# Kernel optimization log

Hardware: AMD Instinct MI355X
Metric: run time of the kernel (lower is better)

## Reference

```python
import jax, jax.numpy as jnp
import numpy as np

B, S, D_IN, D_E, H = 512, 100, 300, 150, 2  # batch, patches, patch feat, embed half, heads
L = S + 1  # 101 tokens with class token
EPS = 1e-5


def setup_inputs() -> dict:
    key = jax.random.key(0)
    ks = jax.random.split(key, 12)
    r = lambda k, shp, s=0.02: (jax.random.normal(k, shp, jnp.float32) * s)
    return {
        "x": jax.random.normal(ks[0], (B, S, D_IN), jnp.float32),
        "Wp": r(ks[1], (D_IN, D_E)), "bp": jnp.zeros((D_E,), jnp.float32),
        "pos_table": r(ks[2], (L, D_E), 1.0),
        "class_embed": r(ks[3], (D_E,), 1.0),
        "Wq": r(ks[4], (H, 2 * D_E, 2 * D_E)),
        "Wk": r(ks[5], (H, 2 * D_E, 2 * D_E)),
        "Wv": r(ks[6], (H, 2 * D_E, 2 * D_E)),
        "bn1_g": jnp.ones((L,), jnp.float32), "bn1_b": jnp.zeros((L,), jnp.float32),
        "Wp1": r(ks[7], (900, 300)), "bp1": jnp.zeros((300,), jnp.float32),
        "bn2_g": jnp.ones((L,), jnp.float32), "bn2_b": jnp.zeros((L,), jnp.float32),
        "fc1_W": r(ks[8], (1200, 512)), "fc1_b": jnp.zeros((512,), jnp.float32),
        "fc2_W": r(ks[9], (512, 2)), "fc2_b": jnp.zeros((2,), jnp.float32),
    }


def _batchnorm(x, g, b):
    # torch BatchNorm1d(101) on [B, 101, F]: normalize per channel (dim 1) over (B, F), training-mode batch stats
    mean = jnp.mean(x, axis=(0, 2), keepdims=True)
    var = jnp.var(x, axis=(0, 2), keepdims=True)
    return (x - mean) * jax.lax.rsqrt(var + EPS) * g[None, :, None] + b[None, :, None]


def reference(x, Wp, bp, pos_table, class_embed, Wq, Wk, Wv, bn1_g, bn1_b,
              Wp1, bp1, bn2_g, bn2_b, fc1_W, fc1_b, fc2_W, fc2_b):
    h = jax.nn.relu(x @ Wp + bp)                                   # [B,100,150]
    cls = jnp.concatenate([jnp.broadcast_to(class_embed, (B, D_E)),
                           jnp.broadcast_to(pos_table[0], (B, D_E))], axis=-1)   # [B,300]
    tok = jnp.concatenate([h, jnp.broadcast_to(pos_table[1:], (B, S, D_E))], axis=-1)  # [B,100,300]
    z = jnp.concatenate([cls[:, None, :], tok], axis=1)            # [B,101,300]
    skip1 = jax.lax.stop_gradient(z)                               # x.clone().detach()

    # multi-head self-attention (per-head Q/K/V, no 1/sqrt(d) scaling, matching source)
    Q = jnp.einsum('bsd,hde->hbse', z, Wq)                         # [H,B,101,300]
    K = jnp.einsum('bsd,hde->hbse', z, Wk)
    V = jnp.einsum('bsd,hde->hbse', z, Wv)
    attn = jax.nn.softmax(jnp.einsum('hbse,hbte->hbst', Q, K), axis=-1)  # [H,B,101,101]
    o = jnp.einsum('hbst,hbte->hbse', attn, V)                     # [H,B,101,300]
    msa = jnp.transpose(o, (1, 2, 0, 3)).reshape(B, L, H * 2 * D_E)  # concat heads -> [B,101,600]

    y = _batchnorm(msa, bn1_g, bn1_b)
    y = jnp.concatenate([y, skip1], axis=-1)                       # [B,101,900]
    skip2 = jax.lax.stop_gradient(y)
    y = jax.nn.relu(y @ Wp1 + bp1)                                 # [B,101,300]
    y = _batchnorm(y, bn2_g, bn2_b)
    y = jnp.concatenate([y, skip2], axis=-1)                       # [B,101,1200]
    out = (y[:, 0, :] @ fc1_W + fc1_b) @ fc2_W + fc2_b             # [B,2]
    return out
```

## Files before the change

### kernel.cpp

```cpp
#include <hip/hip_runtime.h>
#include <hip/hip_fp16.h>
#include <math.h>

#define BB 512
#define SS 100
#define DE 150
#define DM 300
#define LL 101
#define NH 2

typedef _Float16 f16x8 __attribute__((ext_vector_type(8)));
typedef float f32x4 __attribute__((ext_vector_type(4)));

#define WS_CLS    0
#define WS_QK     320
#define WS_S0     960
#define WS_CPOS   964
#define WS_CVEC   1200
#define WS_COLSUM 1536
#define WS_CST0   1856
#define WS_STATS  1860
#define WS_G      2176
#define WS_P3     5248
#define WS_PART1  14336
#define WS_PART2  15360
#define WS_MSA    16384
#define WS_Y1     (WS_MSA + 512*600)
#define WS_WPF    477184
#define WS_WVF    502784
#define WS_ZB16   605184
#define WS_Q0P    769024

__global__ void kC1(const float* __restrict__ pos, const float* __restrict__ cle,
                    const float* __restrict__ Wq, const float* __restrict__ Wp1,
                    const float* __restrict__ Wp, const float* __restrict__ Wv,
                    const float* __restrict__ f1W, const float* __restrict__ f2W,
                    const float* __restrict__ f1b, const float* __restrict__ f2b,
                    float* __restrict__ ws) {
  __shared__ float cls[DM];
  int b = blockIdx.x, tid = threadIdx.x;
  if (b < 35) {
    for (int i = tid; i < DM; i += 256) cls[i] = (i < DE) ? cle[i] : pos[i - DE];
    __syncthreads();
  }
  if (b < 20) {
    int p = b >> 1, h = b & 1;
    const float* wqh = Wq + h * DM * DM;
    int d0 = p * 30;
    for (int e = tid; e < DM; e += 256) {
      float acc = 0.f;
#pragma unroll
      for (int d = 0; d < 30; ++d) acc += cls[d0 + d] * wqh[(d0 + d) * DM + e];
      ws[WS_Q0P + p * 600 + h * 300 + e] = acc;
    }
  } else if (b < 35) {
    int kb = b - 20;
    for (int n = tid; n < DM; n += 256) {
      float cs = 0.f, cv = 0.f;
      for (int k = kb * 60; k < kb * 60 + 60; ++k) {
        float w = Wp1[k * 300 + n];
        if (k < 600) cs += w; else cv += cls[k - 600] * w;
      }
      ws[WS_P3 + kb * 600 + n] = cs;
      ws[WS_P3 + kb * 600 + 300 + n] = cv;
    }
  } else if (b == 35) {
    for (int i = tid; i < DM; i += 256)
      ws[WS_CLS + i] = (i < DE) ? cle[i] : pos[i - DE];
  } else if (b < 111) {
    int wave = tid >> 6, lane = tid & 63;
    int kbase = (b - 36) * 16 + wave * 4;
#pragma unroll
    for (int j = 0; j < 4; ++j) {
      int k = kbase + j;
      const float* r = f1W + k * 512;
      float a0 = 0.f, a1 = 0.f;
      for (int m = lane; m < 512; m += 64) {
        float a = r[m];
        float2 f2 = *(const float2*)&f2W[m * 2];
        a0 += a * f2.x; a1 += a * f2.y;
      }
      for (int o = 32; o; o >>= 1) { a0 += __shfl_xor(a0, o); a1 += __shfl_xor(a1, o); }
      if (!lane) { ws[WS_G + k * 2] = a0; ws[WS_G + k * 2 + 1] = a1; }
    }
  } else if (b == 111) {
    int wave = tid >> 6, lane = tid & 63;
    if (wave < 2) {
      float acc = 0.f;
      for (int m = lane; m < 512; m += 64) acc += f1b[m] * f2W[m * 2 + wave];
      for (int o = 32; o; o >>= 1) acc += __shfl_xor(acc, o);
      if (!lane) ws[WS_CST0 + wave] = f2b[wave] + acc;
    }
  } else if (b < 137) {
    int idx = (b - 112) * 256 + tid;
    int kq = idx / 160, n = idx % 160;
    f16x8 pk;
#pragma unroll
    for (int j = 0; j < 8; ++j) {
      int k = kq * 8 + j;
      float v = (k < DM && n < DE) ? Wp[k * DE + n] : 0.f;
      pk[j] = (_Float16)v;
    }
    *(f16x8*)((char*)ws + (size_t)WS_WPF * 4 + (size_t)idx * 16) = pk;
  } else {
    int idx = (b - 137) * 256 + tid;
    int h = idx / 12800, rem = idx % 12800;
    int kq = rem / 320, n = rem % 320;
    f16x8 pk;
#pragma unroll
    for (int j = 0; j < 8; ++j) {
      int k = kq * 8 + j;
      float v = (k < DM && n < DM) ? Wv[h * DM * DM + k * DM + n] : 0.f;
      pk[j] = (_Float16)v;
    }
    *(f16x8*)((char*)ws + (size_t)WS_WVF * 4 + (size_t)idx * 16) = pk;
  }
}

__global__ void kC2p(const float* __restrict__ Wk, const float* __restrict__ bp1,
                     float* __restrict__ ws) {
  int b = blockIdx.x, tid = threadIdx.x;
  if (b == 150) {
    for (int n = tid; n < DM; n += 256) {
      float cs = 0.f, cv = bp1[n];
      for (int p = 0; p < 15; ++p) {
        cs += ws[WS_P3 + p * 600 + n];
        cv += ws[WS_P3 + p * 600 + 300 + n];
      }
      ws[WS_COLSUM + n] = cs;
      ws[WS_CVEC + n] = cv;
    }
    return;
  }
  __shared__ float q0s[NH * DM];
  for (int i = tid; i < NH * DM; i += 256) {
    float s = 0.f;
#pragma unroll
    for (int p = 0; p < 10; ++p) s += ws[WS_Q0P + p * 600 + i];
    q0s[i] = s;
  }
  __syncthreads();
  int wave = tid >> 6, lane = tid & 63;
  int idx = b * 4 + wave;
  int h = idx / DM, d = idx % DM;
  const float* w = Wk + h * DM * DM + d * DM;
  const float* q = q0s + h * DM;
  float acc = 0.f;
  for (int e = lane; e < DM; e += 64) acc += w[e] * q[e];
  for (int o = 32; o; o >>= 1) acc += __shfl_xor(acc, o);
  if (!lane) ws[WS_QK + idx] = acc;
}

__global__ void kC3(const float* __restrict__ pos, float* __restrict__ ws) {
  int b = blockIdx.x, tid = threadIdx.x;
  int wave = tid >> 6, lane = tid & 63;
  if (b < 50) {
    int idx = b * 4 + wave;
    int tt = idx >> 1, h = idx & 1;
    const float* pr = pos + (tt + 1) * DE;
    const float* qk = ws + WS_QK + h * DM + DE;
    float acc = 0.f;
    for (int j = lane; j < DE; j += 64) acc += pr[j] * qk[j];
    for (int o = 32; o; o >>= 1) acc += __shfl_xor(acc, o);
    if (!lane) ws[WS_CPOS + idx] = acc;
  } else {
    if (wave < NH) {
      float acc = 0.f;
      for (int d = lane; d < DM; d += 64) acc += ws[WS_CLS + d] * ws[WS_QK + wave * DM + d];
      for (int o = 32; o; o >>= 1) acc += __shfl_xor(acc, o);
      if (!lane) ws[WS_S0 + wave] = acc;
    }
  }
}

__launch_bounds__(512, 2)
__global__ void kA(const float* __restrict__ x, const float* __restrict__ bp,
                   const float* __restrict__ pos, float* __restrict__ ws) {
  __shared__ __align__(16) char smem[59520];
  _Float16* xsb = (_Float16*)smem;
  __half (*hb)[DE + 2] = (__half(*)[DE + 2])(smem + 24000);
  float* aux = (float*)(smem + 54400);

  int b = blockIdx.x, tid = threadIdx.x;
  int w = tid >> 6, lane = tid & 63;
  int l16 = lane & 15, lg = lane >> 4;
  int wm = w >> 2, wn = w & 3;
  int nnt = (wn < 3) ? 3 : 1;
  int nt0 = (wn < 3) ? wn * 3 : 9;

  const float* xb = x + b * (SS * DM);
  const _Float16* wpfh = (const _Float16*)((const char*)ws + (size_t)WS_WPF * 4);
  int rowl[4];
#pragma unroll
  for (int mt = 0; mt < 4; ++mt) {
    int r = wm * 64 + mt * 16 + l16;
    rowl[mt] = (r < SS) ? r : (SS - 1);
  }

  f32x4 acc[4][3];
#pragma unroll
  for (int mt = 0; mt < 4; ++mt)
#pragma unroll
    for (int nti = 0; nti < 3; ++nti) acc[mt][nti] = (f32x4){0.f, 0.f, 0.f, 0.f};

  float xrA[4][2], xrB[4][2];

#define XLOAD2(S, XR)                                                          \
  { int kc_ = (S) * 32;                                                        \
    _Pragma("unroll")                                                          \
    for (int i_ = 0; i_ < 4; ++i_) {                                           \
      int t_ = tid + 512 * i_;                                                 \
      if (t_ < 1600) {                                                         \
        int r_ = t_ >> 4, c_ = t_ & 15, k_ = kc_ + 2 * c_;                     \
        if (k_ + 1 < DM) {                                                     \
          float2 v_ = *(const float2*)(xb + r_ * DM + k_);                     \
          XR[i_][0] = v_.x; XR[i_][1] = v_.y;                                  \
        } else {                                                               \
          XR[i_][0] = (k_ < DM) ? xb[r_ * DM + k_] : 0.f;                      \
          XR[i_][1] = 0.f;                                                     \
        } } } }

#define XWRITE2(XP, XR)                                                        \
  { _Pragma("unroll")                                                          \
    for (int i_ = 0; i_ < 4; ++i_) {                                           \
      int t_ = tid + 512 * i_;                                                 \
      if (t_ < 1600) {                                                         \
        int r_ = t_ >> 4, c_ = t_ & 15;                                        \
        *(__half2*)((char*)(XP) + r_ * 80 + c_ * 4) =                          \
            __floats2half2_rn(XR[i_][0], XR[i_][1]);                           \
      } } }

  XLOAD2(0, xrA);
  XWRITE2(xsb, xrA);
  XLOAD2(1, xrB);
  __syncthreads();

  _Float16* bufs[3] = {xsb, xsb + 4000, xsb + 8000};
  for (int s = 0; s < 10; ++s) {
    _Float16* rd = bufs[s % 3];
    _Float16* wr = bufs[(s + 1) % 3];
    if (s < 8) {
      if (s & 1) { XLOAD2(s + 2, xrB); } else { XLOAD2(s + 2, xrA); }
    }
    f16x8 Bf[3];
#pragma unroll
    for (int nti = 0; nti < 3; ++nti)
      if (nti < nnt)
        Bf[nti] = *(const f16x8*)(wpfh +
            ((size_t)(s * 4 + lg) * 160 + (nt0 + nti) * 16 + l16) * 8);
#pragma unroll
    for (int mt = 0; mt < 4; ++mt) {
      f16x8 Af = *(const f16x8*)(rd + rowl[mt] * 40 + lg * 8);
#pragma unroll
      for (int nti = 0; nti < 3; ++nti)
        if (nti < nnt)
          acc[mt][nti] = __builtin_amdgcn_mfma_f32_16x16x32_f16(Af, Bf[nti], acc[mt][nti], 0, 0, 0);
    }
    if (s < 9) {
      if (s & 1) { XWRITE2(wr, xrA); } else { XWRITE2(wr, xrB); }
    }
    __syncthreads();
  }

#pragma unroll
  for (int nti = 0; nti < 3; ++nti) {
    if (nti < nnt) {
      int col = (nt0 + nti) * 16 + l16;
      float bpv = (col < DE) ? bp[col] : 0.f;
#pragma unroll
      for (int mt = 0; mt < 4; ++mt) {
        int rbase = wm * 64 + mt * 16 + lg * 4;
        f32x4 v = acc[mt][nti];
#pragma unroll
        for (int reg = 0; reg < 4; ++reg) {
          int row = rbase + reg;
          if (row < SS && col < DE) {
            float hv = v[reg] + bpv;
            hb[row][col] = __float2half(hv > 0.f ? hv : 0.f);
          }
        }
      }
    }
  }
  for (int i = tid; i < DM; i += 512) {
    aux[i] = ws[WS_QK + (i / DE) * DM + (i % DE)];
    aux[DM + i] = ws[WS_CLS + i];
  }
  __syncthreads();

  if (tid < NH * SS) {
    int hh = tid / SS, tt = tid % SS;
    const __half2* hr = (const __half2*)&hb[tt][0];
    const float* qr = &aux[hh * DE];
    float sa = 0.f, sb = 0.f;
    for (int j2 = 0; j2 < 74; j2 += 2) {
      float2 h0 = __half22float2(hr[j2]);
      float2 q0 = *(const float2*)&qr[2 * j2];
      float2 h1 = __half22float2(hr[j2 + 1]);
      float2 q1 = *(const float2*)&qr[2 * j2 + 2];
      sa += h0.x * q0.x + h0.y * q0.y;
      sb += h1.x * q1.x + h1.y * q1.y;
    }
    {
      float2 h0 = __half22float2(hr[74]);
      float2 q0 = *(const float2*)&qr[148];
      sa += h0.x * q0.x + h0.y * q0.y;
    }
    aux[600 + hh * LL + tt + 1] = sa + sb + ws[WS_CPOS + tt * NH + hh];
  } else if (tid < NH * SS + NH) {
    int hh = tid - NH * SS;
    aux[600 + hh * LL] = ws[WS_S0 + hh];
  }
  __syncthreads();

  if (w < NH) {
    float v0 = aux[600 + w * LL + lane];
    float v1 = (lane + 64 < LL) ? aux[600 + w * LL + lane + 64] : -1e30f;
    float m = fmaxf(v0, v1);
    for (int o = 32; o; o >>= 1) m = fmaxf(m, __shfl_xor(m, o));
    float e0 = expf(v0 - m);
    float e1 = (lane + 64 < LL) ? expf(v1 - m) : 0.f;
    float s = e0 + e1;
    for (int o = 32; o; o >>= 1) s += __shfl_xor(s, o);
    float inv = 1.f / s;
    aux[802 + w * LL + lane] = e0 * inv;
    if (lane + 64 < LL) aux[802 + w * LL + lane + 64] = e1 * inv;
  }
  __syncthreads();

  __half* zb16 = (__half*)((char*)ws + (size_t)WS_ZB16 * 4);
  for (int o = tid; o < NH * DM; o += 512) {
    int hh = o / DM, d = o % DM;
    const float* p = &aux[802 + hh * LL];
    float accA = p[0] * aux[DM + d], accB = 0.f;
    if (d < DE) {
      for (int t = 1; t < 100; t += 2) {
        accA += p[t] * __half2float(hb[t - 1][d]);
        accB += p[t + 1] * __half2float(hb[t][d]);
      }
    } else {
      int dd = d - DE;
      for (int t = 1; t < 100; t += 2) {
        accA += p[t] * pos[t * DE + dd];
        accB += p[t + 1] * pos[(t + 1) * DE + dd];
      }
    }
    zb16[((size_t)hh * 512 + b) * 320 + d] = __float2half(accA + accB);
  }
  if (tid < 40) {
    int hh = tid / 20, dd = 300 + tid % 20;
    zb16[((size_t)hh * 512 + b) * 320 + dd] = __float2half(0.f);
  }
}

__launch_bounds__(512, 4)
__global__ void kV(float* __restrict__ ws) {
  __shared__ float shp[2][8];
  int blk = blockIdx.x;
  int mtile = blk >> 2, nb = (blk >> 1) & 1, h = blk & 1;
  int tid = threadIdx.x;
  int w = tid >> 6, lane = tid & 63;
  int l16 = lane & 15, lg = lane >> 4;
  int wm = w >> 2, wn = w & 3;
  int nnt = (wn < 3) ? 3 : 1;
  int nt0 = (wn < 3) ? wn * 3 : 9;
  int mbase = mtile * 128;

  const __half* zb16 = (const __half*)((const char*)ws + (size_t)WS_ZB16 * 4) + (size_t)h * 512 * 320;
  const __half* wvf  = (const __half*)((const char*)ws + (size_t)WS_WVF * 4) + (size_t)h * 40 * 320 * 8;

  int brow[4];
#pragma unroll
  for (int mt = 0; mt < 4; ++mt) brow[mt] = mbase + wm * 64 + mt * 16 + l16;

  f32x4 acc[4][3];
#pragma unroll
  for (int mt = 0; mt < 4; ++mt)
#pragma unroll
    for (int nti = 0; nti < 3; ++nti) acc[mt][nti] = (f32x4){0.f, 0.f, 0.f, 0.f};

  for (int s = 0; s < 10; ++s) {
    f16x8 Bf[3];
#pragma unroll
    for (int nti = 0; nti < 3; ++nti)
      if (nti < nnt) {
        int n = nb * 160 + (nt0 + nti) * 16 + l16;
        Bf[nti] = *(const f16x8*)&wvf[((size_t)(s * 4 + lg) * 320 + n) * 8];
      }
#pragma unroll
    for (int mt = 0; mt < 4; ++mt) {
      f16x8 Af = *(const f16x8*)&zb16[(size_t)brow[mt] * 320 + s * 32 + lg * 8];
#pragma unroll
      for (int nti = 0; nti < 3; ++nti)
        if (nti < nnt)
          acc[mt][nti] = __builtin_amdgcn_mfma_f32_16x16x32_f16(Af, Bf[nti], acc[mt][nti], 0, 0, 0);
    }
  }

  float s_ = 0.f, ss_ = 0.f;
#pragma unroll
  for (int nti = 0; nti < 3; ++nti) {
    if (nti < nnt) {
      int col = nb * 160 + (nt0 + nti) * 16 + l16;
      if (col < DM) {
#pragma unroll
        for (int mt = 0; mt < 4; ++mt) {
          int rbase = mbase + wm * 64 + mt * 16 + lg * 4;
          f32x4 v = acc[mt][nti];
#pragma unroll
          for (int reg = 0; reg < 4; ++reg) {
            int row = rbase + reg;
            float val = v[reg];
            ws[WS_MSA + row * 600 + h * DM + col] = val;
            s_ += val; ss_ += val * val;
          }
        }
      }
    }
  }
  for (int o = 32; o; o >>= 1) { s_ += __shfl_xor(s_, o); ss_ += __shfl_xor(ss_, o); }
  if (!lane) { shp[0][w] = s_; shp[1][w] = ss_; }
  __syncthreads();
  if (!tid) {
    float S = 0.f, SS2 = 0.f;
    for (int i = 0; i < 8; ++i) { S += shp[0][i]; SS2 += shp[1][i]; }
    ws[WS_PART1 + blk * 2] = S;
    ws[WS_PART1 + blk * 2 + 1] = SS2;
  }
}

__launch_bounds__(512)
__global__ void k5(const float* __restrict__ Wp1, const float* __restrict__ g1,
                   const float* __restrict__ b1, float* __restrict__ ws) {
  __shared__ float ab[2][600];
  __shared__ float part[2][2][300];
  __shared__ float sh[2][8];
  __shared__ float s_a1, s_b1;
  int b0 = blockIdx.x * 2, tid = threadIdx.x;
  int wv = tid >> 6, ln = tid & 63;
  for (int i = tid; i < 1200; i += 512) ab[i / 600][i % 600] = ws[WS_MSA + b0 * 600 + i];
  {
    float s = 0.f, ss = 0.f;
    if (tid < 16) { s = ws[WS_PART1 + tid * 2]; ss = ws[WS_PART1 + tid * 2 + 1]; }
    for (int o = 32; o; o >>= 1) { s += __shfl_xor(s, o); ss += __shfl_xor(ss, o); }
    if (!ln) { sh[0][wv] = s; sh[1][wv] = ss; }
  }
  __syncthreads();
  if (!tid) {
    float S = 0.f, SS2 = 0.f;
    for (int i = 0; i < 8; ++i) { S += sh[0][i]; SS2 += sh[1][i]; }
    float n = (float)(BB * 600);
    float mean = S / n, var = SS2 / n - mean * mean;
    float a = (1.f / sqrtf(var + 1e-5f)) * g1[0];
    s_a1 = a; s_b1 = b1[0] - a * mean;
    if (blockIdx.x == 0) { ws[WS_STATS + 0] = a; ws[WS_STATS + 1] = s_b1; }
  }
  __syncthreads();
  int g = tid >> 8, t = tid & 255;
  int kbeg = g * 300, kend = kbeg + 300;
  for (int n = t; n < 300; n += 256) {
    float a0 = 0.f, a1v = 0.f;
    for (int k = kbeg; k < kend; ++k) {
      float wq = Wp1[k * 300 + n];
      a0 += ab[0][k] * wq;
      a1v += ab[1][k] * wq;
    }
    part[g][0][n] = a0;
    part[g][1][n] = a1v;
  }
  __syncthreads();
  float a1 = s_a1, beta1 = s_b1;
  float s2 = 0.f, ss2 = 0.f;
  for (int n = tid; n < 300; n += 512) {
    float c = beta1 * ws[WS_COLSUM + n] + ws[WS_CVEC + n];
    float v0 = a1 * (part[0][0][n] + part[1][0][n]) + c;
    float v1 = a1 * (part[0][1][n] + part[1][1][n]) + c;
    v0 = v0 > 0.f ? v0 : 0.f;
    v1 = v1 > 0.f ? v1 : 0.f;
    ws[WS_Y1 + b0 * 300 + n] = v0;
    ws[WS_Y1 + (b0 + 1) * 300 + n] = v1;
    s2 += v0 + v1; ss2 += v0 * v0 + v1 * v1;
  }
  for (int o = 32; o; o >>= 1) { s2 += __shfl_xor(s2, o); ss2 += __shfl_xor(ss2, o); }
  if (!ln) { sh[0][wv] = s2; sh[1][wv] = ss2; }
  __syncthreads();
  if (!tid) {
    float S = 0.f, SS2 = 0.f;
    for (int i = 0; i < 8; ++i) { S += sh[0][i]; SS2 += sh[1][i]; }
    ws[WS_PART2 + blockIdx.x * 2] = S;
    ws[WS_PART2 + blockIdx.x * 2 + 1] = SS2;
  }
}

__launch_bounds__(256)
__global__ void k7(const float* __restrict__ g2, const float* __restrict__ b2,
                   float* __restrict__ out, const float* __restrict__ ws) {
  __shared__ float Gs[2400];
  __shared__ float sh[2][4];
  __shared__ float cc[4];
  int tid = threadIdx.x, wv = tid >> 6, ln = tid & 63;
  for (int i = tid; i < 2400; i += 256) Gs[i] = ws[WS_G + i];
  {
    float s = ws[WS_PART2 + tid * 2], ss = ws[WS_PART2 + tid * 2 + 1];
    for (int o = 32; o; o >>= 1) { s += __shfl_xor(s, o); ss += __shfl_xor(ss, o); }
    if (!ln) { sh[0][wv] = s; sh[1][wv] = ss; }
  }
  __syncthreads();
  if (!tid) {
    float S = 0.f, SS2 = 0.f;
    for (int i = 0; i < 4; ++i) { S += sh[0][i]; SS2 += sh[1][i]; }
    float n = (float)(BB * 300);
    float mean = S / n, var = SS2 / n - mean * mean;
    float a = (1.f / sqrtf(var + 1e-5f)) * g2[0];
    cc[0] = a; cc[1] = b2[0] - a * mean;
  }
  __syncthreads();
  if (tid < 2) {
    int c = tid;
    float sg1 = 0.f, sg2 = 0.f, sg3 = 0.f;
    for (int k = 0; k < 300; ++k) sg1 += Gs[k * 2 + c];
    for (int k = 300; k < 900; ++k) sg2 += Gs[k * 2 + c];
    for (int j = 0; j < 300; ++j) sg3 += ws[WS_CLS + j] * Gs[(900 + j) * 2 + c];
    cc[2 + c] = ws[WS_CST0 + c] + sg3 + cc[1] * sg1 + ws[WS_STATS + 1] * sg2;
  }
  __syncthreads();
  int b = blockIdx.x * 4 + wv;
  float a1 = ws[WS_STATS + 0], a2 = cc[0];
  const float* y1 = ws + WS_Y1 + b * 300;
  const float* ms = ws + WS_MSA + b * 600;
  float o0 = 0.f, o1 = 0.f, p0 = 0.f, p1 = 0.f;
  for (int k = ln; k < 300; k += 64) { float v = y1[k]; o0 += v * Gs[k * 2]; o1 += v * Gs[k * 2 + 1]; }
  for (int j = ln; j < 600; j += 64) { float v = ms[j]; p0 += v * Gs[(300 + j) * 2]; p1 += v * Gs[(300 + j) * 2 + 1]; }
  for (int o = 32; o; o >>= 1) {
    o0 += __shfl_xor(o0, o); o1 += __shfl_xor(o1, o);
    p0 += __shfl_xor(p0, o); p1 += __shfl_xor(p1, o);
  }
  if (!ln) {
    out[b * 2] = a2 * o0 + a1 * p0 + cc[2];
    out[b * 2 + 1] = a2 * o1 + a1 * p1 + cc[3];
  }
}

extern "C" void kernel_launch(void* const* d_in, const int* in_sizes, int n_in,
                              void* d_out, int out_size, void* d_ws, size_t ws_size,
                              hipStream_t stream) {
  const float* x    = (const float*)d_in[0];
  const float* Wp   = (const float*)d_in[1];
  const float* bp   = (const float*)d_in[2];
  const float* pos  = (const float*)d_in[3];
  const float* cle  = (const float*)d_in[4];
  const float* Wq   = (const float*)d_in[5];
  const float* Wk   = (const float*)d_in[6];
  const float* Wv   = (const float*)d_in[7];
  const float* bn1g = (const float*)d_in[8];
  const float* bn1b = (const float*)d_in[9];
  const float* Wp1  = (const float*)d_in[10];
  const float* bp1  = (const float*)d_in[11];
  const float* bn2g = (const float*)d_in[12];
  const float* bn2b = (const float*)d_in[13];
  const float* f1W  = (const float*)d_in[14];
  const float* f1b  = (const float*)d_in[15];
  const float* f2W  = (const float*)d_in[16];
  const float* f2b  = (const float*)d_in[17];
  float* ws = (float*)d_ws;
  float* out = (float*)d_out;

  hipLaunchKernelGGL(kC1, dim3(237), dim3(256), 0, stream, pos, cle, Wq, Wp1, Wp, Wv, f1W, f2W, f1b, f2b, ws);
  hipLaunchKernelGGL(kC2p, dim3(151), dim3(256), 0, stream, Wk, bp1, ws);
  hipLaunchKernelGGL(kC3, dim3(51), dim3(256), 0, stream, pos, ws);
  hipLaunchKernelGGL(kA, dim3(512), dim3(512), 0, stream, x, bp, pos, ws);
  hipLaunchKernelGGL(kV, dim3(16), dim3(512), 0, stream, ws);
  hipLaunchKernelGGL(k5, dim3(256), dim3(512), 0, stream, Wp1, bn1g, bn1b, ws);
  hipLaunchKernelGGL(k7, dim3(128), dim3(256), 0, stream, bn2g, bn2b, out, ws);
}
```

Baseline: 128.8 us.

## Load x fragments directly from global memory instead of LDS triple-buffering

The patch-projection GEMM in kA now has each lane read its A fragments straight from global memory as float4 pairs and convert them to fp16 in registers. This replaces the register-prefetch plus LDS triple-buffer pipeline and removes the per-step __syncthreads. Shared memory shrinks, so launch bounds ask for 4 blocks per CU to raise occupancy. The cost is redundant global reads, since the 4 column-group waves sharing a row block each load the same x rows, and there is no explicit prefetch, so latency hiding relies on occupancy.

After: 130.3 us. About the same (+1.2%).

```diff
diff --git a/kernel.cpp b/kernel.cpp
--- a/kernel.cpp
+++ b/kernel.cpp
@@ -173,13 +173,12 @@
   }
 }
 
-__launch_bounds__(512, 2)
+__launch_bounds__(512, 4)
 __global__ void kA(const float* __restrict__ x, const float* __restrict__ bp,
                    const float* __restrict__ pos, float* __restrict__ ws) {
-  __shared__ __align__(16) char smem[59520];
-  _Float16* xsb = (_Float16*)smem;
-  __half (*hb)[DE + 2] = (__half(*)[DE + 2])(smem + 24000);
-  float* aux = (float*)(smem + 54400);
+  __shared__ __align__(16) char smem[35520];
+  __half (*hb)[DE + 2] = (__half(*)[DE + 2])smem;
+  float* aux = (float*)(smem + 30400);
 
   int b = blockIdx.x, tid = threadIdx.x;
   int w = tid >> 6, lane = tid & 63;
@@ -203,63 +202,53 @@
 #pragma unroll
     for (int nti = 0; nti < 3; ++nti) acc[mt][nti] = (f32x4){0.f, 0.f, 0.f, 0.f};
 
-  float xrA[4][2], xrB[4][2];
-
-#define XLOAD2(S, XR)                                                          \
-  { int kc_ = (S) * 32;                                                        \
-    _Pragma("unroll")                                                          \
-    for (int i_ = 0; i_ < 4; ++i_) {                                           \
-      int t_ = tid + 512 * i_;                                                 \
-      if (t_ < 1600) {                                                         \
-        int r_ = t_ >> 4, c_ = t_ & 15, k_ = kc_ + 2 * c_;                     \
-        if (k_ + 1 < DM) {                                                     \
-          float2 v_ = *(const float2*)(xb + r_ * DM + k_);                     \
-          XR[i_][0] = v_.x; XR[i_][1] = v_.y;                                  \
-        } else {                                                               \
-          XR[i_][0] = (k_ < DM) ? xb[r_ * DM + k_] : 0.f;                      \
-          XR[i_][1] = 0.f;                                                     \
-        } } } }
-
-#define XWRITE2(XP, XR)                                                        \
-  { _Pragma("unroll")                                                          \
-    for (int i_ = 0; i_ < 4; ++i_) {                                           \
-      int t_ = tid + 512 * i_;                                                 \
-      if (t_ < 1600) {                                                         \
-        int r_ = t_ >> 4, c_ = t_ & 15;                                        \
-        *(__half2*)((char*)(XP) + r_ * 80 + c_ * 4) =                          \
-            __floats2half2_rn(XR[i_][0], XR[i_][1]);                           \
-      } } }
-
-  XLOAD2(0, xrA);
-  XWRITE2(xsb, xrA);
-  XLOAD2(1, xrB);
-  __syncthreads();
-
-  _Float16* bufs[3] = {xsb, xsb + 4000, xsb + 8000};
-  for (int s = 0; s < 10; ++s) {
-    _Float16* rd = bufs[s % 3];
-    _Float16* wr = bufs[(s + 1) % 3];
-    if (s < 8) {
-      if (s & 1) { XLOAD2(s + 2, xrB); } else { XLOAD2(s + 2, xrA); }
-    }
+  for (int s = 0; s < 9; ++s) {
     f16x8 Bf[3];
 #pragma unroll
     for (int nti = 0; nti < 3; ++nti)
       if (nti < nnt)
         Bf[nti] = *(const f16x8*)(wpfh +
             ((size_t)(s * 4 + lg) * 160 + (nt0 + nti) * 16 + l16) * 8);
+    int k0 = s * 32 + lg * 8;
 #pragma unroll
     for (int mt = 0; mt < 4; ++mt) {
-      f16x8 Af = *(const f16x8*)(rd + rowl[mt] * 40 + lg * 8);
+      const float* xr = xb + rowl[mt] * DM + k0;
+      float4 q0 = *(const float4*)xr;
+      float4 q1 = *(const float4*)(xr + 4);
+      f16x8 Af;
+      Af[0] = (_Float16)q0.x; Af[1] = (_Float16)q0.y;
+      Af[2] = (_Float16)q0.z; Af[3] = (_Float16)q0.w;
+      Af[4] = (_Float16)q1.x; Af[5] = (_Float16)q1.y;
+      Af[6] = (_Float16)q1.z; Af[7] = (_Float16)q1.w;
 #pragma unroll
       for (int nti = 0; nti < 3; ++nti)
         if (nti < nnt)
           acc[mt][nti] = __builtin_amdgcn_mfma_f32_16x16x32_f16(Af, Bf[nti], acc[mt][nti], 0, 0, 0);
     }
-    if (s < 9) {
-      if (s & 1) { XWRITE2(wr, xrA); } else { XWRITE2(wr, xrB); }
-    }
-    __syncthreads();
+  }
+  {
+    const int s = 9;
+    f16x8 Bf[3];
+#pragma unroll
+    for (int nti = 0; nti < 3; ++nti)
+      if (nti < nnt)
+        Bf[nti] = *(const f16x8*)(wpfh +
+            ((size_t)(s * 4 + lg) * 160 + (nt0 + nti) * 16 + l16) * 8);
+    int k0 = s * 32 + lg * 8;
+#pragma unroll
+    for (int mt = 0; mt < 4; ++mt) {
+      const float* xr = xb + rowl[mt] * DM;
+      f16x8 Af;
+#pragma unroll
+      for (int j = 0; j < 8; ++j) {
+        int k = k0 + j;
+        Af[j] = (k < DM) ? (_Float16)xr[k] : (_Float16)0.f;
+      }
+#pragma unroll
+      for (int nti = 0; nti < 3; ++nti)
+        if (nti < nnt)
+          acc[mt][nti] = __builtin_amdgcn_mfma_f32_16x16x32_f16(Af, Bf[nti], acc[mt][nti], 0, 0, 0);
+    }
   }
 
 #pragma unroll
```
